# Kernel tuning notes

Hardware: AMD Instinct MI355X
Metric: run time of the kernel (lower is better)

## Reference

```python
import jax, jax.numpy as jnp
import numpy as np
import math

D_MODEL = 256
NUM_SLOTS = 128
RANK = 32
STEPS = 6
VOCAB = 32000
SEQ = 512
BATCH = 8
LN_EPS = 1e-5


def setup_inputs() -> dict:
    key = jax.random.key(0)
    ks = jax.random.split(key, 16)
    std = 0.02
    inp = {
        "input_ids": jax.random.randint(ks[0], (BATCH, SEQ), 0, VOCAB),
        "attention_mask": jnp.ones((BATCH, SEQ), dtype=jnp.int32),
        "token_emb": jax.random.normal(ks[1], (VOCAB, D_MODEL), jnp.float32) * std,
        "pos_emb": jax.random.normal(ks[2], (SEQ, D_MODEL), jnp.float32) * std,
        "H": jax.random.normal(ks[3], (NUM_SLOTS, D_MODEL), jnp.float32) / math.sqrt(D_MODEL),
        "W_source": jax.random.normal(ks[4], (NUM_SLOTS, NUM_SLOTS, D_MODEL, RANK), jnp.float32) * std,
        "W_target": jax.random.normal(ks[5], (NUM_SLOTS, NUM_SLOTS, RANK, D_MODEL), jnp.float32) * std,
        "Wq_in": jax.random.normal(ks[6], (D_MODEL, D_MODEL), jnp.float32) / math.sqrt(D_MODEL),
        "Wk_slots": jax.random.normal(ks[7], (D_MODEL, D_MODEL), jnp.float32) / math.sqrt(D_MODEL),
        "Wv_in": jax.random.normal(ks[8], (D_MODEL, D_MODEL), jnp.float32) / math.sqrt(D_MODEL),
        "Wq_out": jax.random.normal(ks[9], (D_MODEL, D_MODEL), jnp.float32) / math.sqrt(D_MODEL),
        "Wk_fin": jax.random.normal(ks[10], (D_MODEL, D_MODEL), jnp.float32) / math.sqrt(D_MODEL),
        "Wv_fin": jax.random.normal(ks[11], (D_MODEL, D_MODEL), jnp.float32) / math.sqrt(D_MODEL),
        "W_out_proj": jax.random.normal(ks[12], (VOCAB, D_MODEL), jnp.float32) / math.sqrt(D_MODEL),
        "ln_scale": jnp.ones((STEPS, D_MODEL), jnp.float32),
        "ln_bias": jnp.zeros((STEPS, D_MODEL), jnp.float32),
    }
    return inp


def _layernorm(x, g, b):
    mu = jnp.mean(x, axis=-1, keepdims=True)
    var = jnp.var(x, axis=-1, keepdims=True)
    return (x - mu) / jnp.sqrt(var + LN_EPS) * g + b


def _forward(input_ids, attention_mask, token_emb, pos_emb, H, W_source, W_target,
             Wq_in, Wk_slots, Wv_in, Wq_out, Wk_fin, Wv_fin, W_out_proj, ln_scale, ln_bias):
    B, L = input_ids.shape
    scale = 1.0 / math.sqrt(D_MODEL)
    # embeddings (dropout is identity in eval)
    X = token_emb[input_ids] + pos_emb[jnp.arange(L)][None]  # (B,L,D)
    # compress: input tokens -> slots
    Q_in = X @ Wq_in.T                      # (B,L,D)
    K_sl = H @ Wk_slots.T                   # (S,D)
    V_in = X @ Wv_in.T                      # (B,L,D)
    A = jax.nn.softmax(Q_in @ K_sl.T * scale, axis=-1)  # (B,L,S)
    m = attention_mask.astype(A.dtype)[..., None]
    A = A * m
    A = A / (jnp.sum(A, axis=1, keepdims=True) + 1e-8)
    IR = jnp.einsum('bls,bld->bsd', A, V_in)            # (B,S,D)
    H_state = H[None] + IR                               # (B,S,D)

    off_diag = (1.0 - jnp.eye(NUM_SLOTS, dtype=H_state.dtype))  # (S,S)

    def step(h, lnp):
        g, b = lnp
        # bilinear slot-to-slot influence; contract directly, no (B,S,S,D) expand of h
        inter = jnp.einsum('bid,ijdr->bijr', h, W_source)        # (B,S,S,R)
        out = jnp.einsum('bijr,ijrd->bijd', inter, W_target)     # (B,S,S,D)
        infl = jnp.einsum('bijd,ij->bjd', out, off_diag)         # mask diag + sum over i
        h = _layernorm(h + jax.nn.relu(infl), g, b)
        return h, None

    H_state, _ = jax.lax.scan(step, H_state, (ln_scale, ln_bias))

    # expand: slots -> tokens
    Q_out = X @ Wq_out.T                   # (B,L,D)
    K_f = H_state @ Wk_fin.T               # (B,S,D)
    V_f = H_state @ Wv_fin.T               # (B,S,D)
    A2 = jax.nn.softmax(jnp.einsum('bld,bsd->bls', Q_out, K_f) * scale, axis=-1)
    Y = jnp.einsum('bls,bsd->bld', A2, V_f)
    logits = Y @ W_out_proj.T              # (B,L,V)
    return logits


def reference(input_ids, attention_mask, token_emb, pos_emb, H, W_source, W_target,
              Wq_in, Wk_slots, Wv_in, Wq_out, Wk_fin, Wv_fin, W_out_proj, ln_scale, ln_bias):
    return _forward(input_ids, attention_mask, token_emb, pos_emb, H, W_source, W_target,
                    Wq_in, Wk_slots, Wv_in, Wq_out, Wk_fin, Wv_fin, W_out_proj, ln_scale, ln_bias)
```

## Files before the change

kernel.cpp:

```cpp
#include <hip/hip_runtime.h>
#include <hip/hip_bf16.h>
#include <math.h>

#define D_MODEL 256
#define NUM_SLOTS 128
#define RANK 32
#define N_STEPS 6
#define VOCAB 32000
#define SEQ 512
#define BATCH 8
#define NTOK (BATCH*SEQ)
#define LN_EPS 1e-5f
#define SM_SCALE 0.0625f
#define IGROUPS 8
#define IPG (NUM_SLOTS/IGROUPS)

typedef __attribute__((ext_vector_type(8))) short bf16x8;
typedef __attribute__((ext_vector_type(8))) _Float16 f16x8;
typedef __attribute__((ext_vector_type(4))) float f32x4;

#define GLD_LDS16(g, l) __builtin_amdgcn_global_load_lds( \
    (const __attribute__((address_space(1))) unsigned int*)(g), \
    (__attribute__((address_space(3))) unsigned int*)(l), 16, 0, 0)

__device__ inline unsigned short f2bf(float x) {
    unsigned u = __float_as_uint(x);
    unsigned r = u + 0x7fff + ((u >> 16) & 1);
    return (unsigned short)(r >> 16);
}
__device__ inline float bf2f(unsigned short h) {
    return __uint_as_float(((unsigned)h) << 16);
}
__device__ inline unsigned pk2(float a, float b) {
    auto v = __builtin_amdgcn_cvt_pkrtz(a, b);
    union { decltype(v) x; unsigned u; } c;
    c.x = v;
    return c.u;
}
__device__ inline unsigned short f2h(float x) {
    union { _Float16 h; unsigned short u; } c;
    c.h = (_Float16)x;
    return c.u;
}

__global__ __launch_bounds__(256) void k_embed(const int* __restrict__ ids,
        const float* __restrict__ tok, const float* __restrict__ pos,
        float* __restrict__ X) {
    int bl = blockIdx.x;
    int d  = threadIdx.x;
    int l  = bl % SEQ;
    int id = ids[bl];
    X[(size_t)bl*D_MODEL + d] = tok[(size_t)id*D_MODEL + d] + pos[l*D_MODEL + d];
}

__global__ __launch_bounds__(256) void k_gemm_nt(const float* __restrict__ A,
        const float* __restrict__ B, float* __restrict__ C, int M, int N, int K) {
    __shared__ float As[32][64];
    __shared__ float Bs[32][64];
    int bm = blockIdx.x * 64, bn = blockIdx.y * 64;
    int t = threadIdx.x;
    int tm = (t & 15) * 4, tn = (t >> 4) * 4;
    float acc[4][4] = {};
    for (int k0 = 0; k0 < K; k0 += 32) {
        #pragma unroll
        for (int r = 0; r < 8; ++r) {
            int idx = r*256 + t;
            int m = idx >> 5, k = idx & 31;
            As[k][m] = A[(size_t)(bm+m)*K + k0 + k];
        }
        #pragma unroll
        for (int r = 0; r < 8; ++r) {
            int idx = r*256 + t;
            int n = idx >> 5, k = idx & 31;
            Bs[k][n] = B[(size_t)(bn+n)*K + k0 + k];
        }
        __syncthreads();
        #pragma unroll
        for (int k = 0; k < 32; ++k) {
            float4 a4 = *(const float4*)&As[k][tm];
            float4 b4 = *(const float4*)&Bs[k][tn];
            float a[4] = {a4.x,a4.y,a4.z,a4.w};
            float b[4] = {b4.x,b4.y,b4.z,b4.w};
            #pragma unroll
            for (int i = 0; i < 4; ++i)
                #pragma unroll
                for (int jj = 0; jj < 4; ++jj)
                    acc[i][jj] += a[i]*b[jj];
        }
        __syncthreads();
    }
    #pragma unroll
    for (int i = 0; i < 4; ++i) {
        float4 v = make_float4(acc[i][0],acc[i][1],acc[i][2],acc[i][3]);
        *(float4*)&C[(size_t)(bm+tm+i)*N + bn+tn] = v;
    }
}

__global__ __launch_bounds__(256) void k_split(const float* __restrict__ in,
        unsigned short* __restrict__ hi, unsigned short* __restrict__ lo, int n4) {
    int i = blockIdx.x*256 + threadIdx.x;
    if (i >= n4) return;
    float4 v = ((const float4*)in)[i];
    float f[4] = {v.x, v.y, v.z, v.w};
    ushort4 h, lw;
    unsigned short* hp = &h.x; unsigned short* lp = &lw.x;
    #pragma unroll
    for (int j = 0; j < 4; ++j) {
        unsigned short hb = f2bf(f[j]);
        hp[j] = hb;
        lp[j] = f2bf(f[j] - bf2f(hb));
    }
    ((ushort4*)hi)[i] = h;
    ((ushort4*)lo)[i] = lw;
}

__global__ __launch_bounds__(256) void k_logits(
        const unsigned short* __restrict__ Ahg, const unsigned short* __restrict__ Alg,
        const unsigned short* __restrict__ Bhg, const unsigned short* __restrict__ Blg,
        float* __restrict__ C) {
    __shared__ short lds[4*128*64];
    short* Ah = lds;
    short* Al = lds + 8192;
    short* Bh = lds + 16384;
    short* Bl = lds + 24576;
    int bm = blockIdx.x * 128, bn = blockIdx.y * 128;
    int t = threadIdx.x;
    int w = t >> 6, l = t & 63;
    int wr = w >> 1, wc = w & 1;
    int lr = l & 15, lk = l >> 4;
    f32x4 acc[4][4];
    #pragma unroll
    for (int mi = 0; mi < 4; ++mi)
        #pragma unroll
        for (int ni = 0; ni < 4; ++ni)
            acc[mi][ni] = (f32x4){0.f,0.f,0.f,0.f};

    for (int kc = 0; kc < 4; ++kc) {
        #pragma unroll
        for (int i = 0; i < 4; ++i) {
            int v = t + i*256;
            int row = v >> 3, cv = v & 7;
            int so = row*64 + ((cv ^ (row & 7)) << 3);
            size_t ga = (size_t)(bm+row)*256 + kc*64 + cv*8;
            size_t gb = (size_t)(bn+row)*256 + kc*64 + cv*8;
            *(bf16x8*)&Ah[so] = *(const bf16x8*)&Ahg[ga];
            *(bf16x8*)&Al[so] = *(const bf16x8*)&Alg[ga];
            *(bf16x8*)&Bh[so] = *(const bf16x8*)&Bhg[gb];
            *(bf16x8*)&Bl[so] = *(const bf16x8*)&Blg[gb];
        }
        __syncthreads();
        #pragma unroll
        for (int s = 0; s < 2; ++s) {
            bf16x8 ah[4], al[4], bh[4], bl[4];
            #pragma unroll
            for (int mi = 0; mi < 4; ++mi) {
                int row = wr*64 + mi*16 + lr;
                int off = row*64 + ((((s<<2)+lk) ^ (row&7)) << 3);
                ah[mi] = *(bf16x8*)&Ah[off];
                al[mi] = *(bf16x8*)&Al[off];
            }
            #pragma unroll
            for (int ni = 0; ni < 4; ++ni) {
                int row = wc*64 + ni*16 + lr;
                int off = row*64 + ((((s<<2)+lk) ^ (row&7)) << 3);
                bh[ni] = *(bf16x8*)&Bh[off];
                bl[ni] = *(bf16x8*)&Bl[off];
            }
            #pragma unroll
            for (int mi = 0; mi < 4; ++mi)
                #pragma unroll
                for (int ni = 0; ni < 4; ++ni) {
                    acc[mi][ni] = __builtin_amdgcn_mfma_f32_16x16x32_bf16(ah[mi], bh[ni], acc[mi][ni], 0, 0, 0);
                    acc[mi][ni] = __builtin_amdgcn_mfma_f32_16x16x32_bf16(ah[mi], bl[ni], acc[mi][ni], 0, 0, 0);
                    acc[mi][ni] = __builtin_amdgcn_mfma_f32_16x16x32_bf16(al[mi], bh[ni], acc[mi][ni], 0, 0, 0);
                }
        }
        __syncthreads();
    }
    #pragma unroll
    for (int mi = 0; mi < 4; ++mi)
        #pragma unroll
        for (int ni = 0; ni < 4; ++ni) {
            int col = bn + wc*64 + ni*16 + lr;
            #pragma unroll
            for (int r = 0; r < 4; ++r) {
                int row = bm + wr*64 + mi*16 + lk*4 + r;
                C[(size_t)row*VOCAB + col] = acc[mi][ni][r];
            }
        }
}

__global__ __launch_bounds__(128) void k_softmax_mask(float* __restrict__ A,
        const int* __restrict__ mask) {
    int row = blockIdx.x;
    int s = threadIdx.x;
    __shared__ float red[128];
    float v = A[(size_t)row*NUM_SLOTS + s] * SM_SCALE;
    red[s] = v; __syncthreads();
    for (int o = 64; o > 0; o >>= 1) { if (s < o) red[s] = fmaxf(red[s], red[s+o]); __syncthreads(); }
    float mx = red[0]; __syncthreads();
    float e = expf(v - mx);
    red[s] = e; __syncthreads();
    for (int o = 64; o > 0; o >>= 1) { if (s < o) red[s] += red[s+o]; __syncthreads(); }
    float sum = red[0];
    float m = (float)mask[row];
    A[(size_t)row*NUM_SLOTS + s] = e / sum * m;
}

__global__ __launch_bounds__(128) void k_colsum(const float* __restrict__ A,
        float* __restrict__ cs) {
    int b = blockIdx.x; int s = threadIdx.x;
    const float* Ab = A + (size_t)b*SEQ*NUM_SLOTS + s;
    float acc = 0.f;
    for (int l = 0; l < SEQ; ++l) acc += Ab[(size_t)l*NUM_SLOTS];
    cs[b*NUM_SLOTS + s] = acc + 1e-8f;
}

__global__ __launch_bounds__(256) void k_ir(const float* __restrict__ A,
        const float* __restrict__ V, const float* __restrict__ H,
        const float* __restrict__ cs, float* __restrict__ Hs,
        unsigned short* __restrict__ Hs16) {
    int bs = blockIdx.x; int b = bs >> 7; int s = bs & 127;
    int d = threadIdx.x;
    float inv = 1.0f / cs[bs];
    const float* Ab = A + (size_t)b*SEQ*NUM_SLOTS + s;
    const float* Vb = V + (size_t)b*SEQ*D_MODEL + d;
    float acc = 0.f;
    for (int l = 0; l < SEQ; ++l) acc += Ab[(size_t)l*NUM_SLOTS] * Vb[(size_t)l*D_MODEL];
    float v = H[s*D_MODEL + d] + acc * inv;
    Hs[(size_t)bs*D_MODEL + d] = v;
    Hs16[(size_t)bs*D_MODEL + d] = f2h(v);
}

__global__ __launch_bounds__(256) void k_convert_s(const float* __restrict__ Ws,
        unsigned short* __restrict__ WF) {
    int i = blockIdx.x, j = blockIdx.y, hf = blockIdx.z;
    int t = threadIdx.x;
    __shared__ float lds[128*33];
    size_t sBase = ((size_t)i*128 + j)*8192;
    size_t pOut = ((size_t)j*128 + i)*16384;
    const float4* s4 = (const float4*)(Ws + sBase) + hf*1024;
    #pragma unroll
    for (int p = 0; p < 4; ++p) {
        int f4 = p*256 + t;
        float4 v = s4[f4];
        *(float4*)&lds[(f4 >> 3)*33 + 4*(f4 & 7)] = v;
    }
    __syncthreads();
    bool diag = (i == j);
    #pragma unroll
    for (int q = 0; q < 2; ++q) {
        int cl = q*256 + t;
        int ksl = cl >> 7, mt = (cl >> 6) & 1, l = cl & 63;
        int g = l >> 4, c = l & 15;
        union { f16x8 v; } o;
        #pragma unroll
        for (int e = 0; e < 8; ++e) {
            float f = diag ? 0.f : lds[(ksl*32 + g*8 + e)*33 + mt*16 + c];
            o.v[e] = (_Float16)f;
        }
        *(f16x8*)(WF + pOut + (size_t)hf*4096 + (size_t)cl*8) = o.v;
    }
}

__global__ __launch_bounds__(256) void k_convert_t(const float* __restrict__ Wt,
        unsigned short* __restrict__ WF) {
    int i = blockIdx.x, j = blockIdx.y, hf = blockIdx.z;
    int t = threadIdx.x;
    __shared__ float lds[32*133];
    size_t sBase = ((size_t)i*128 + j)*8192;
    size_t pOut = ((size_t)j*128 + i)*16384;
    const float4* s4 = (const float4*)(Wt + sBase);
    #pragma unroll
    for (int p = 0; p < 4; ++p) {
        int idx = p*256 + t;
        int r = idx >> 5, c4 = idx & 31;
        float4 v = s4[r*64 + hf*32 + c4];
        *(float4*)&lds[r*133 + c4*4] = v;
    }
    __syncthreads();
    #pragma unroll
    for (int q = 0; q < 2; ++q) {
        int cl = q*256 + t;
        int ntl = cl >> 6, l = cl & 63;
        int g = l >> 4, c = l & 15;
        union { f16x8 v; } o;
        #pragma unroll
        for (int e = 0; e < 8; ++e)
            o.v[e] = (_Float16)lds[(g*8 + e)*133 + ntl*16 + c];
        *(f16x8*)(WF + pOut + 8192 + (size_t)hf*4096 + (size_t)cl*8) = o.v;
    }
}

__global__ __launch_bounds__(256, 4) void k_pairs_mfma(const unsigned short* __restrict__ h16,
        const unsigned short* __restrict__ WF, float* __restrict__ part) {
    __shared__ unsigned short lds[2*10240];
    int j = blockIdx.x, g = blockIdx.y;
    int t = threadIdx.x, w = t >> 6, l = t & 63;
    int lg = l >> 4, c = l & 15;
    const unsigned short* pbase = WF + ((size_t)j*128 + g*16)*16384;

    {
        const unsigned short* src = pbase;
        #pragma unroll
        for (int q = 0; q < 4; ++q)
            GLD_LDS16(src + (size_t)(q*256 + t)*8, &lds[(q*256 + t)*8]);
        const unsigned short* hsrc = h16 + ((size_t)(t&7)*NUM_SLOTS + g*16)*D_MODEL + (t>>3)*8;
        GLD_LDS16(hsrc, &lds[8192 + t*8]);
    }
    __builtin_amdgcn_sched_barrier(0);
    f16x8 bqn[4];
    #pragma unroll
    for (int nt = 0; nt < 4; ++nt)
        bqn[nt] = *(const f16x8*)(pbase + 8192 + (size_t)((w*4+nt)*64 + l)*8);
    __builtin_amdgcn_sched_barrier(0);

    f32x4 acc[4];
    #pragma unroll
    for (int nt = 0; nt < 4; ++nt) acc[nt] = (f32x4){0.f,0.f,0.f,0.f};
    f16x8 hzero;
    #pragma unroll
    for (int e = 0; e < 8; ++e) hzero[e] = (_Float16)0.f;

    #pragma unroll 2
    for (int ii = 0; ii < 16; ++ii) {
        int cur = ii & 1;
        asm volatile("s_waitcnt vmcnt(4) lgkmcnt(0)" ::: "memory");
        __builtin_amdgcn_s_barrier();
        __builtin_amdgcn_sched_barrier(0);
        if (ii < 15) {
            const unsigned short* src = pbase + (size_t)(ii+1)*16384;
            unsigned short* dst = &lds[(cur^1)*10240];
            #pragma unroll
            for (int q = 0; q < 4; ++q)
                GLD_LDS16(src + (size_t)(q*256 + t)*8, dst + (size_t)(q*256 + t)*8);
            const unsigned short* hsrc = h16 + ((size_t)(t&7)*NUM_SLOTS + (g*16+ii+1))*D_MODEL + (t>>3)*8;
            GLD_LDS16(hsrc, dst + 8192 + (size_t)t*8);
        }
        __builtin_amdgcn_sched_barrier(0);
        f16x8 bq[4];
        #pragma unroll
        for (int nt = 0; nt < 4; ++nt) bq[nt] = bqn[nt];
        if (ii < 15) {
            const unsigned short* bp = pbase + (size_t)(ii+1)*16384 + 8192;
            #pragma unroll
            for (int nt = 0; nt < 4; ++nt)
                bqn[nt] = *(const f16x8*)(bp + (size_t)((w*4+nt)*64 + l)*8);
        }
        const unsigned short* buf = &lds[cur*10240];
        f32x4 d1[2];
        d1[0] = (f32x4){0.f,0.f,0.f,0.f};
        d1[1] = (f32x4){0.f,0.f,0.f,0.f};
        #pragma unroll
        for (int ks = 0; ks < 8; ++ks) {
            f16x8 a0 = *(const f16x8*)(buf + (size_t)((ks*2+0)*64 + l)*8);
            f16x8 a1 = *(const f16x8*)(buf + (size_t)((ks*2+1)*64 + l)*8);
            f16x8 hv = *(const f16x8*)(buf + 8192 + (size_t)(((ks*4+lg)*8 + (c&7)))*8);
            f16x8 hb = (c < 8) ? hv : hzero;
            d1[0] = __builtin_amdgcn_mfma_f32_16x16x32_f16(a0, hb, d1[0], 0, 0, 0);
            d1[1] = __builtin_amdgcn_mfma_f32_16x16x32_f16(a1, hb, d1[1], 0, 0, 0);
        }
        unsigned q0 = pk2(d1[0][0], d1[0][1]);
        unsigned q1 = pk2(d1[0][2], d1[0][3]);
        unsigned s0 = pk2(d1[1][0], d1[1][1]);
        unsigned s1 = pk2(d1[1][2], d1[1][3]);
        int srcLo = 32*(lg & 1) + c;
        int srcHi = srcLo + 16;
        unsigned a0s = (unsigned)__shfl((int)q0, srcLo, 64);
        unsigned a1s = (unsigned)__shfl((int)q1, srcLo, 64);
        unsigned a2s = (unsigned)__shfl((int)q0, srcHi, 64);
        unsigned a3s = (unsigned)__shfl((int)q1, srcHi, 64);
        unsigned b0s = (unsigned)__shfl((int)s0, srcLo, 64);
        unsigned b1s = (unsigned)__shfl((int)s1, srcLo, 64);
        unsigned b2s = (unsigned)__shfl((int)s0, srcHi, 64);
        unsigned b3s = (unsigned)__shfl((int)s1, srcHi, 64);
        bool himt = ((lg >> 1) & 1);
        union { unsigned u[4]; f16x8 v; } A2u;
        A2u.u[0] = himt ? b0s : a0s;
        A2u.u[1] = himt ? b1s : a1s;
        A2u.u[2] = himt ? b2s : a2s;
        A2u.u[3] = himt ? b3s : a3s;
        #pragma unroll
        for (int nt = 0; nt < 4; ++nt)
            acc[nt] = __builtin_amdgcn_mfma_f32_16x16x32_f16(A2u.v, bq[nt], acc[nt], 0, 0, 0);
    }
    if (lg < 2) {
        #pragma unroll
        for (int nt = 0; nt < 4; ++nt) {
            int d = (w*4 + nt)*16 + c;
            #pragma unroll
            for (int r = 0; r < 4; ++r) {
                int b = lg*4 + r;
                part[(((size_t)g*BATCH + b)*NUM_SLOTS + j)*D_MODEL + d] = acc[nt][r];
            }
        }
    }
}

__global__ __launch_bounds__(256) void k_pairs(const float* __restrict__ h,
        const float* __restrict__ Ws, const float* __restrict__ Wt,
        float* __restrict__ part) {
    int j = blockIdx.x;
    int g = blockIdx.y;
    int t = threadIdx.x;
    __shared__ float sh_h[BATCH][D_MODEL];
    __shared__ float sh_inter[BATCH][RANK];
    float acc[BATCH];
    #pragma unroll
    for (int b = 0; b < BATCH; ++b) acc[b] = 0.f;
    int tb = t >> 5, tr = t & 31;
    for (int ii = 0; ii < IPG; ++ii) {
        int i = g*IPG + ii;
        if (i == j) continue;
        #pragma unroll
        for (int b = 0; b < BATCH; ++b)
            sh_h[b][t] = h[((size_t)b*NUM_SLOTS + i)*D_MODEL + t];
        __syncthreads();
        const float* ws = Ws + ((size_t)i*NUM_SLOTS + j)*(D_MODEL*RANK);
        float accA = 0.f;
        #pragma unroll 8
        for (int d = 0; d < D_MODEL; ++d)
            accA += sh_h[tb][d] * ws[(size_t)d*RANK + tr];
        sh_inter[tb][tr] = accA;
        __syncthreads();
        const float* wt = Wt + ((size_t)i*NUM_SLOTS + j)*(RANK*D_MODEL);
        #pragma unroll 8
        for (int r = 0; r < RANK; ++r) {
            float w = wt[(size_t)r*D_MODEL + t];
            #pragma unroll
            for (int b = 0; b < BATCH; ++b) acc[b] += sh_inter[b][r] * w;
        }
        __syncthreads();
    }
    #pragma unroll
    for (int b = 0; b < BATCH; ++b)
        part[(((size_t)g*BATCH + b)*NUM_SLOTS + j)*D_MODEL + t] = acc[b];
}

__global__ __launch_bounds__(256) void k_ln(float* __restrict__ h,
        unsigned short* __restrict__ h16, const float* __restrict__ part,
        const float* __restrict__ gma, const float* __restrict__ bta) {
    int bj = blockIdx.x;
    int t = threadIdx.x;
    int b = bj >> 7, j = bj & 127;
    __shared__ float red[256];
    float v = 0.f;
    #pragma unroll
    for (int g = 0; g < IGROUPS; ++g)
        v += part[(((size_t)g*BATCH + b)*NUM_SLOTS + j)*D_MODEL + t];
    float x = h[(size_t)bj*D_MODEL + t] + fmaxf(v, 0.f);
    red[t] = x; __syncthreads();
    for (int o = 128; o > 0; o >>= 1) { if (t < o) red[t] += red[t+o]; __syncthreads(); }
    float mu = red[0] * (1.0f/D_MODEL); __syncthreads();
    float dx = x - mu;
    red[t] = dx*dx; __syncthreads();
    for (int o = 128; o > 0; o >>= 1) { if (t < o) red[t] += red[t+o]; __syncthreads(); }
    float var = red[0] * (1.0f/D_MODEL);
    float outv = dx * rsqrtf(var + LN_EPS) * gma[t] + bta[t];
    h[(size_t)bj*D_MODEL + t] = outv;
    h16[(size_t)bj*D_MODEL + t] = f2h(outv);
}

__global__ __launch_bounds__(128) void k_attn2(const float* __restrict__ Q,
        const float* __restrict__ Kf, float* __restrict__ A2) {
    int bl = blockIdx.x; int b = bl / SEQ;
    int s = threadIdx.x;
    __shared__ float q[D_MODEL];
    __shared__ float red[128];
    q[s]       = Q[(size_t)bl*D_MODEL + s];
    q[s + 128] = Q[(size_t)bl*D_MODEL + s + 128];
    __syncthreads();
    const float* kf = Kf + ((size_t)b*NUM_SLOTS + s)*D_MODEL;
    float acc = 0.f;
    #pragma unroll 8
    for (int d = 0; d < D_MODEL; ++d) acc += q[d]*kf[d];
    acc *= SM_SCALE;
    red[s] = acc; __syncthreads();
    for (int o = 64; o > 0; o >>= 1) { if (s < o) red[s] = fmaxf(red[s], red[s+o]); __syncthreads(); }
    float mx = red[0]; __syncthreads();
    float e = expf(acc - mx);
    red[s] = e; __syncthreads();
    for (int o = 64; o > 0; o >>= 1) { if (s < o) red[s] += red[s+o]; __syncthreads(); }
    A2[(size_t)bl*NUM_SLOTS + s] = e / red[0];
}

__global__ __launch_bounds__(256) void k_y(const float* __restrict__ A2,
        const float* __restrict__ Vf, unsigned short* __restrict__ Yh,
        unsigned short* __restrict__ Yl) {
    int bl = blockIdx.x; int b = bl / SEQ;
    int d = threadIdx.x;
    const float* a = A2 + (size_t)bl*NUM_SLOTS;
    const float* v = Vf + (size_t)b*NUM_SLOTS*D_MODEL + d;
    float acc = 0.f;
    #pragma unroll 4
    for (int s = 0; s < NUM_SLOTS; ++s) acc += a[s]*v[(size_t)s*D_MODEL];
    unsigned short hb = f2bf(acc);
    Yh[(size_t)bl*D_MODEL + d] = hb;
    Yl[(size_t)bl*D_MODEL + d] = f2bf(acc - bf2f(hb));
}

extern "C" void kernel_launch(void* const* d_in, const int* in_sizes, int n_in,
                              void* d_out, int out_size, void* d_ws, size_t ws_size,
                              hipStream_t stream) {
    const int*   ids    = (const int*)d_in[0];
    const int*   amask  = (const int*)d_in[1];
    const float* tok    = (const float*)d_in[2];
    const float* pos    = (const float*)d_in[3];
    const float* Hin    = (const float*)d_in[4];
    const float* Ws     = (const float*)d_in[5];
    const float* Wt     = (const float*)d_in[6];
    const float* Wq_in  = (const float*)d_in[7];
    const float* Wk_sl  = (const float*)d_in[8];
    const float* Wv_in  = (const float*)d_in[9];
    const float* Wq_out = (const float*)d_in[10];
    const float* Wk_fin = (const float*)d_in[11];
    const float* Wv_fin = (const float*)d_in[12];
    const float* Wop    = (const float*)d_in[13];
    const float* lnsc   = (const float*)d_in[14];
    const float* lnbs   = (const float*)d_in[15];
    float* out = (float*)d_out;

    const size_t WF_USH = (size_t)16384 * 16384;
    const size_t F32_FLOATS = 18580480ULL;
    const bool useF16 = ws_size >= WF_USH*2 + F32_FLOATS*4 + 256;

    unsigned short* WF = (unsigned short*)d_ws;
    float* ws = useF16 ? (float*)(WF + WF_USH) : (float*)d_ws;

    float* X    = ws;
    float* Qin  = X    + (size_t)NTOK*D_MODEL;
    float* Vin  = Qin  + (size_t)NTOK*D_MODEL;
    float* Ksl  = Vin  + (size_t)NTOK*D_MODEL;
    float* Asc  = Ksl  + (size_t)NUM_SLOTS*D_MODEL;
    float* cs   = Asc  + (size_t)NTOK*NUM_SLOTS;
    float* Hst  = cs   + (size_t)BATCH*NUM_SLOTS;
    float* part = Hst  + (size_t)BATCH*NUM_SLOTS*D_MODEL;
    float* Qout = part + (size_t)IGROUPS*BATCH*NUM_SLOTS*D_MODEL;
    float* Kf   = Qout + (size_t)NTOK*D_MODEL;
    float* Vf   = Kf   + (size_t)BATCH*NUM_SLOTS*D_MODEL;
    float* A2   = Vf   + (size_t)BATCH*NUM_SLOTS*D_MODEL;
    float* Yb   = A2   + (size_t)NTOK*NUM_SLOTS;
    unsigned short* Yh = (unsigned short*)(Yb + (size_t)NTOK*D_MODEL);
    unsigned short* Yl = Yh + (size_t)NTOK*D_MODEL;
    unsigned short* Wh = Yl + (size_t)NTOK*D_MODEL;
    unsigned short* Wl = Wh + (size_t)VOCAB*D_MODEL;
    unsigned short* Hst16 = Wl + (size_t)VOCAB*D_MODEL;

    if (useF16) {
        k_convert_s<<<dim3(128, 128, 2), 256, 0, stream>>>(Ws, WF);
        k_convert_t<<<dim3(128, 128, 2), 256, 0, stream>>>(Wt, WF);
    }
    k_split<<<(VOCAB*D_MODEL/4 + 255)/256, 256, 0, stream>>>(Wop, Wh, Wl, VOCAB*D_MODEL/4);

    k_embed<<<NTOK, 256, 0, stream>>>(ids, tok, pos, X);
    k_gemm_nt<<<dim3(NTOK/64, 4), 256, 0, stream>>>(X, Wq_in, Qin, NTOK, D_MODEL, D_MODEL);
    k_gemm_nt<<<dim3(2, 4),       256, 0, stream>>>(Hin, Wk_sl, Ksl, NUM_SLOTS, D_MODEL, D_MODEL);
    k_gemm_nt<<<dim3(NTOK/64, 4), 256, 0, stream>>>(X, Wv_in, Vin, NTOK, D_MODEL, D_MODEL);
    k_gemm_nt<<<dim3(NTOK/64, 2), 256, 0, stream>>>(Qin, Ksl, Asc, NTOK, NUM_SLOTS, D_MODEL);
    k_softmax_mask<<<NTOK, 128, 0, stream>>>(Asc, amask);
    k_colsum<<<BATCH, 128, 0, stream>>>(Asc, cs);
    k_ir<<<BATCH*NUM_SLOTS, 256, 0, stream>>>(Asc, Vin, Hin, cs, Hst, Hst16);
    for (int st = 0; st < N_STEPS; ++st) {
        if (useF16)
            k_pairs_mfma<<<dim3(NUM_SLOTS, IGROUPS), 256, 0, stream>>>(Hst16, WF, part);
        else
            k_pairs<<<dim3(NUM_SLOTS, IGROUPS), 256, 0, stream>>>(Hst, Ws, Wt, part);
        k_ln<<<BATCH*NUM_SLOTS, 256, 0, stream>>>(Hst, Hst16, part, lnsc + st*D_MODEL, lnbs + st*D_MODEL);
    }
    k_gemm_nt<<<dim3(NTOK/64, 4), 256, 0, stream>>>(X, Wq_out, Qout, NTOK, D_MODEL, D_MODEL);
    k_gemm_nt<<<dim3(BATCH*NUM_SLOTS/64, 4), 256, 0, stream>>>(Hst, Wk_fin, Kf, BATCH*NUM_SLOTS, D_MODEL, D_MODEL);
    k_gemm_nt<<<dim3(BATCH*NUM_SLOTS/64, 4), 256, 0, stream>>>(Hst, Wv_fin, Vf, BATCH*NUM_SLOTS, D_MODEL, D_MODEL);
    k_attn2<<<NTOK, 128, 0, stream>>>(Qout, Kf, A2);
    k_y<<<NTOK, 256, 0, stream>>>(A2, Vf, Yh, Yl);
    k_logits<<<dim3(NTOK/128, VOCAB/128), 256, 0, stream>>>(Yh, Yl, Wh, Wl, out);
}
```

Baseline: 1.554 ms.

## Use fp16 two-term logits GEMM, fuse input projections, split colsum and unroll reductions

The logits GEMM moves from a three-MFMA bf16 hi/lo split to fp16, with Y split into hi/lo and W_out_proj rounded to a single fp16 copy. This cuts MFMA work by a third and drops one operand's LDS staging and global traffic. The three X projections (Qin, Vin, Qout) now run as one batched launch, and the column sum is split across 8 chunks per batch for more parallelism. The k_ir reduction loops are unrolled with multiple accumulators, and the risk is extra rounding error because W_out_proj loses its low-order correction term.

```diff
diff --git a/kernel.cpp b/kernel.cpp
--- a/kernel.cpp
+++ b/kernel.cpp
@@ -42,6 +42,11 @@
     c.h = (_Float16)x;
     return c.u;
 }
+__device__ inline float h2f(unsigned short u) {
+    union { unsigned short u; _Float16 h; } c;
+    c.u = u;
+    return (float)c.h;
+}
 
 __global__ __launch_bounds__(256) void k_embed(const int* __restrict__ ids,
         const float* __restrict__ tok, const float* __restrict__ pos,
@@ -96,33 +101,71 @@
     }
 }
 
-__global__ __launch_bounds__(256) void k_split(const float* __restrict__ in,
-        unsigned short* __restrict__ hi, unsigned short* __restrict__ lo, int n4) {
+__global__ __launch_bounds__(256) void k_gemm3(const float* __restrict__ A,
+        const float* __restrict__ B0, const float* __restrict__ B1,
+        const float* __restrict__ B2, float* __restrict__ C0,
+        float* __restrict__ C1, float* __restrict__ C2) {
+    const int K = D_MODEL, N = D_MODEL;
+    const float* B = blockIdx.z == 0 ? B0 : (blockIdx.z == 1 ? B1 : B2);
+    float* C = blockIdx.z == 0 ? C0 : (blockIdx.z == 1 ? C1 : C2);
+    __shared__ float As[32][64];
+    __shared__ float Bs[32][64];
+    int bm = blockIdx.x * 64, bn = blockIdx.y * 64;
+    int t = threadIdx.x;
+    int tm = (t & 15) * 4, tn = (t >> 4) * 4;
+    float acc[4][4] = {};
+    for (int k0 = 0; k0 < K; k0 += 32) {
+        #pragma unroll
+        for (int r = 0; r < 8; ++r) {
+            int idx = r*256 + t;
+            int m = idx >> 5, k = idx & 31;
+            As[k][m] = A[(size_t)(bm+m)*K + k0 + k];
+        }
+        #pragma unroll
+        for (int r = 0; r < 8; ++r) {
+            int idx = r*256 + t;
+            int n = idx >> 5, k = idx & 31;
+            Bs[k][n] = B[(size_t)(bn+n)*K + k0 + k];
+        }
+        __syncthreads();
+        #pragma unroll
+        for (int k = 0; k < 32; ++k) {
+            float4 a4 = *(const float4*)&As[k][tm];
+            float4 b4 = *(const float4*)&Bs[k][tn];
+            float a[4] = {a4.x,a4.y,a4.z,a4.w};
+            float b[4] = {b4.x,b4.y,b4.z,b4.w};
+            #pragma unroll
+            for (int i = 0; i < 4; ++i)
+                #pragma unroll
+                for (int jj = 0; jj < 4; ++jj)
+                    acc[i][jj] += a[i]*b[jj];
+        }
+        __syncthreads();
+    }
+    #pragma unroll
+    for (int i = 0; i < 4; ++i) {
+        float4 v = make_float4(acc[i][0],acc[i][1],acc[i][2],acc[i][3]);
+        *(float4*)&C[(size_t)(bm+tm+i)*N + bn+tn] = v;
+    }
+}
+
+__global__ __launch_bounds__(256) void k_split16(const float* __restrict__ in,
+        unsigned short* __restrict__ o, int n4) {
     int i = blockIdx.x*256 + threadIdx.x;
     if (i >= n4) return;
     float4 v = ((const float4*)in)[i];
-    float f[4] = {v.x, v.y, v.z, v.w};
-    ushort4 h, lw;
-    unsigned short* hp = &h.x; unsigned short* lp = &lw.x;
-    #pragma unroll
-    for (int j = 0; j < 4; ++j) {
-        unsigned short hb = f2bf(f[j]);
-        hp[j] = hb;
-        lp[j] = f2bf(f[j] - bf2f(hb));
-    }
-    ((ushort4*)hi)[i] = h;
-    ((ushort4*)lo)[i] = lw;
+    ushort4 h;
+    h.x = f2h(v.x); h.y = f2h(v.y); h.z = f2h(v.z); h.w = f2h(v.w);
+    ((ushort4*)o)[i] = h;
 }
 
 __global__ __launch_bounds__(256) void k_logits(
         const unsigned short* __restrict__ Ahg, const unsigned short* __restrict__ Alg,
-        const unsigned short* __restrict__ Bhg, const unsigned short* __restrict__ Blg,
-        float* __restrict__ C) {
-    __shared__ short lds[4*128*64];
+        const unsigned short* __restrict__ Bhg, float* __restrict__ C) {
+    __shared__ short lds[3*128*64];
     short* Ah = lds;
     short* Al = lds + 8192;
     short* Bh = lds + 16384;
-    short* Bl = lds + 24576;
     int bm = blockIdx.x * 128, bn = blockIdx.y * 128;
     int t = threadIdx.x;
     int w = t >> 6, l = t & 63;
@@ -146,33 +189,30 @@
             *(bf16x8*)&Ah[so] = *(const bf16x8*)&Ahg[ga];
             *(bf16x8*)&Al[so] = *(const bf16x8*)&Alg[ga];
             *(bf16x8*)&Bh[so] = *(const bf16x8*)&Bhg[gb];
-            *(bf16x8*)&Bl[so] = *(const bf16x8*)&Blg[gb];
         }
         __syncthreads();
         #pragma unroll
         for (int s = 0; s < 2; ++s) {
-            bf16x8 ah[4], al[4], bh[4], bl[4];
+            f16x8 ah[4], al[4], bh[4];
             #pragma unroll
             for (int mi = 0; mi < 4; ++mi) {
                 int row = wr*64 + mi*16 + lr;
                 int off = row*64 + ((((s<<2)+lk) ^ (row&7)) << 3);
-                ah[mi] = *(bf16x8*)&Ah[off];
-                al[mi] = *(bf16x8*)&Al[off];
+                ah[mi] = *(f16x8*)&Ah[off];
+                al[mi] = *(f16x8*)&Al[off];
             }
             #pragma unroll
             for (int ni = 0; ni < 4; ++ni) {
                 int row = wc*64 + ni*16 + lr;
                 int off = row*64 + ((((s<<2)+lk) ^ (row&7)) << 3);
-                bh[ni] = *(bf16x8*)&Bh[off];
-                bl[ni] = *(bf16x8*)&Bl[off];
+                bh[ni] = *(f16x8*)&Bh[off];
             }
             #pragma unroll
             for (int mi = 0; mi < 4; ++mi)
                 #pragma unroll
                 for (int ni = 0; ni < 4; ++ni) {
-                    acc[mi][ni] = __builtin_amdgcn_mfma_f32_16x16x32_bf16(ah[mi], bh[ni], acc[mi][ni], 0, 0, 0);
-                    acc[mi][ni] = __builtin_amdgcn_mfma_f32_16x16x32_bf16(ah[mi], bl[ni], acc[mi][ni], 0, 0, 0);
-                    acc[mi][ni] = __builtin_amdgcn_mfma_f32_16x16x32_bf16(al[mi], bh[ni], acc[mi][ni], 0, 0, 0);
+                    acc[mi][ni] = __builtin_amdgcn_mfma_f32_16x16x32_f16(ah[mi], bh[ni], acc[mi][ni], 0, 0, 0);
+                    acc[mi][ni] = __builtin_amdgcn_mfma_f32_16x16x32_f16(al[mi], bh[ni], acc[mi][ni], 0, 0, 0);
                 }
         }
         __syncthreads();
@@ -208,25 +248,40 @@
 }
 
 __global__ __launch_bounds__(128) void k_colsum(const float* __restrict__ A,
-        float* __restrict__ cs) {
-    int b = blockIdx.x; int s = threadIdx.x;
-    const float* Ab = A + (size_t)b*SEQ*NUM_SLOTS + s;
-    float acc = 0.f;
-    for (int l = 0; l < SEQ; ++l) acc += Ab[(size_t)l*NUM_SLOTS];
-    cs[b*NUM_SLOTS + s] = acc + 1e-8f;
+        float* __restrict__ csp) {
+    int b = blockIdx.x; int ch = blockIdx.y; int s = threadIdx.x;
+    const float* Ab = A + ((size_t)b*SEQ + ch*64)*NUM_SLOTS + s;
+    float a0 = 0.f, a1 = 0.f, a2 = 0.f, a3 = 0.f;
+    #pragma unroll
+    for (int l = 0; l < 64; l += 4) {
+        a0 += Ab[(size_t)(l+0)*NUM_SLOTS];
+        a1 += Ab[(size_t)(l+1)*NUM_SLOTS];
+        a2 += Ab[(size_t)(l+2)*NUM_SLOTS];
+        a3 += Ab[(size_t)(l+3)*NUM_SLOTS];
+    }
+    csp[(b*8 + ch)*NUM_SLOTS + s] = (a0+a1) + (a2+a3);
 }
 
 __global__ __launch_bounds__(256) void k_ir(const float* __restrict__ A,
         const float* __restrict__ V, const float* __restrict__ H,
-        const float* __restrict__ cs, float* __restrict__ Hs,
+        const float* __restrict__ csp, float* __restrict__ Hs,
         unsigned short* __restrict__ Hs16) {
     int bs = blockIdx.x; int b = bs >> 7; int s = bs & 127;
     int d = threadIdx.x;
-    float inv = 1.0f / cs[bs];
+    float sum = 1e-8f;
+    #pragma unroll
+    for (int p = 0; p < 8; ++p) sum += csp[(b*8 + p)*NUM_SLOTS + s];
+    float inv = 1.0f / sum;
     const float* Ab = A + (size_t)b*SEQ*NUM_SLOTS + s;
     const float* Vb = V + (size_t)b*SEQ*D_MODEL + d;
-    float acc = 0.f;
-    for (int l = 0; l < SEQ; ++l) acc += Ab[(size_t)l*NUM_SLOTS] * Vb[(size_t)l*D_MODEL];
+    float a0 = 0.f, a1 = 0.f, a2 = 0.f, a3 = 0.f;
+    for (int l = 0; l < SEQ; l += 4) {
+        a0 += Ab[(size_t)(l+0)*NUM_SLOTS] * Vb[(size_t)(l+0)*D_MODEL];
+        a1 += Ab[(size_t)(l+1)*NUM_SLOTS] * Vb[(size_t)(l+1)*D_MODEL];
+        a2 += Ab[(size_t)(l+2)*NUM_SLOTS] * Vb[(size_t)(l+2)*D_MODEL];
+        a3 += Ab[(size_t)(l+3)*NUM_SLOTS] * Vb[(size_t)(l+3)*D_MODEL];
+    }
+    float acc = (a0+a1) + (a2+a3);
     float v = H[s*D_MODEL + d] + acc * inv;
     Hs[(size_t)bs*D_MODEL + d] = v;
     Hs16[(size_t)bs*D_MODEL + d] = f2h(v);
@@ -494,9 +549,9 @@
     float acc = 0.f;
     #pragma unroll 4
     for (int s = 0; s < NUM_SLOTS; ++s) acc += a[s]*v[(size_t)s*D_MODEL];
-    unsigned short hb = f2bf(acc);
-    Yh[(size_t)bl*D_MODEL + d] = hb;
-    Yl[(size_t)bl*D_MODEL + d] = f2bf(acc - bf2f(hb));
+    unsigned short yh = f2h(acc);
+    Yh[(size_t)bl*D_MODEL + d] = yh;
+    Yl[(size_t)bl*D_MODEL + d] = f2h(acc - h2f(yh));
 }
 
 extern "C" void kernel_launch(void* const* d_in, const int* in_sizes, int n_in,
@@ -521,7 +576,7 @@
     float* out = (float*)d_out;
 
     const size_t WF_USH = (size_t)16384 * 16384;
-    const size_t F32_FLOATS = 18580480ULL;
+    const size_t F32_FLOATS = 18600000ULL;
     const bool useF16 = ws_size >= WF_USH*2 + F32_FLOATS*4 + 256;
 
     unsigned short* WF = (unsigned short*)d_ws;
@@ -532,8 +587,8 @@
     float* Vin  = Qin  + (size_t)NTOK*D_MODEL;
     float* Ksl  = Vin  + (size_t)NTOK*D_MODEL;
     float* Asc  = Ksl  + (size_t)NUM_SLOTS*D_MODEL;
-    float* cs   = Asc  + (size_t)NTOK*NUM_SLOTS;
-    float* Hst  = cs   + (size_t)BATCH*NUM_SLOTS;
+    float* csp  = Asc  + (size_t)NTOK*NUM_SLOTS;
+    float* Hst  = csp  + (size_t)BATCH*8*NUM_SLOTS;
     float* part = Hst  + (size_t)BATCH*NUM_SLOTS*D_MODEL;
     float* Qout = part + (size_t)IGROUPS*BATCH*NUM_SLOTS*D_MODEL;
     float* Kf   = Qout + (size_t)NTOK*D_MODEL;
@@ -542,24 +597,22 @@
     float* Yb   = A2   + (size_t)NTOK*NUM_SLOTS;
     unsigned short* Yh = (unsigned short*)(Yb + (size_t)NTOK*D_MODEL);
     unsigned short* Yl = Yh + (size_t)NTOK*D_MODEL;
-    unsigned short* Wh = Yl + (size_t)NTOK*D_MODEL;
-    unsigned short* Wl = Wh + (size_t)VOCAB*D_MODEL;
-    unsigned short* Hst16 = Wl + (size_t)VOCAB*D_MODEL;
+    unsigned short* Wf16 = Yl + (size_t)NTOK*D_MODEL;
+    unsigned short* Hst16 = Wf16 + (size_t)VOCAB*D_MODEL;
 
     if (useF16) {
         k_convert_s<<<dim3(128, 128, 2), 256, 0, stream>>>(Ws, WF);
         k_convert_t<<<dim3(128, 128, 2), 256, 0, stream>>>(Wt, WF);
     }
-    k_split<<<(VOCAB*D_MODEL/4 + 255)/256, 256, 0, stream>>>(Wop, Wh, Wl, VOCAB*D_MODEL/4);
+    k_split16<<<(VOCAB*D_MODEL/4 + 255)/256, 256, 0, stream>>>(Wop, Wf16, VOCAB*D_MODEL/4);
 
     k_embed<<<NTOK, 256, 0, stream>>>(ids, tok, pos, X);
-    k_gemm_nt<<<dim3(NTOK/64, 4), 256, 0, stream>>>(X, Wq_in, Qin, NTOK, D_MODEL, D_MODEL);
-    k_gemm_nt<<<dim3(2, 4),       256, 0, stream>>>(Hin, Wk_sl, Ksl, NUM_SLOTS, D_MODEL, D_MODEL);
-    k_gemm_nt<<<dim3(NTOK/64, 4), 256, 0, stream>>>(X, Wv_in, Vin, NTOK, D_MODEL, D_MODEL);
+    k_gemm3<<<dim3(NTOK/64, 4, 3), 256, 0, stream>>>(X, Wq_in, Wv_in, Wq_out, Qin, Vin, Qout);
+    k_gemm_nt<<<dim3(2, 4), 256, 0, stream>>>(Hin, Wk_sl, Ksl, NUM_SLOTS, D_MODEL, D_MODEL);
     k_gemm_nt<<<dim3(NTOK/64, 2), 256, 0, stream>>>(Qin, Ksl, Asc, NTOK, NUM_SLOTS, D_MODEL);
     k_softmax_mask<<<NTOK, 128, 0, stream>>>(Asc, amask);
-    k_colsum<<<BATCH, 128, 0, stream>>>(Asc, cs);
-    k_ir<<<BATCH*NUM_SLOTS, 256, 0, stream>>>(Asc, Vin, Hin, cs, Hst, Hst16);
+    k_colsum<<<dim3(BATCH, 8), 128, 0, stream>>>(Asc, csp);
+    k_ir<<<BATCH*NUM_SLOTS, 256, 0, stream>>>(Asc, Vin, Hin, csp, Hst, Hst16);
     for (int st = 0; st < N_STEPS; ++st) {
         if (useF16)
             k_pairs_mfma<<<dim3(NUM_SLOTS, IGROUPS), 256, 0, stream>>>(Hst16, WF, part);
@@ -567,10 +620,9 @@
             k_pairs<<<dim3(NUM_SLOTS, IGROUPS), 256, 0, stream>>>(Hst, Ws, Wt, part);
         k_ln<<<BATCH*NUM_SLOTS, 256, 0, stream>>>(Hst, Hst16, part, lnsc + st*D_MODEL, lnbs + st*D_MODEL);
     }
-    k_gemm_nt<<<dim3(NTOK/64, 4), 256, 0, stream>>>(X, Wq_out, Qout, NTOK, D_MODEL, D_MODEL);
     k_gemm_nt<<<dim3(BATCH*NUM_SLOTS/64, 4), 256, 0, stream>>>(Hst, Wk_fin, Kf, BATCH*NUM_SLOTS, D_MODEL, D_MODEL);
     k_gemm_nt<<<dim3(BATCH*NUM_SLOTS/64, 4), 256, 0, stream>>>(Hst, Wv_fin, Vf, BATCH*NUM_SLOTS, D_MODEL, D_MODEL);
     k_attn2<<<NTOK, 128, 0, stream>>>(Qout, Kf, A2);
     k_y<<<NTOK, 256, 0, stream>>>(A2, Vf, Yh, Yl);
-    k_logits<<<dim3(NTOK/128, VOCAB/128), 256, 0, stream>>>(Yh, Yl, Wh, Wl, out);
-}
+    k_logits<<<dim3(NTOK/128, VOCAB/128), 256, 0, stream>>>(Yh, Yl, Wf16, out);
+}
```

After: 1.513 ms. -2.6%, faster.
